# Kernel optimization log

Measured on AMD Instinct MI355X. Metric: run time of the kernel, lower is better.

Reference implementation:

```python
import jax, jax.numpy as jnp
import numpy as np

B, F, D, H = 256, 128, 512, 8
HD = D // H
SPARSITY = 0.5
KVAL = max(1, int(F * SPARSITY))  # 64


def setup_inputs() -> dict:
    key = jax.random.key(0)
    ks = jax.random.split(key, 12)
    s = 0.02
    x = jax.random.normal(ks[0], (B, F, D), dtype=jnp.float32)
    Wq = jax.random.normal(ks[1], (D, D), dtype=jnp.float32) * s
    bq = jnp.zeros((D,), jnp.float32)
    Wk = jax.random.normal(ks[2], (D, D), dtype=jnp.float32) * s
    bk = jnp.zeros((D,), jnp.float32)
    Wv = jax.random.normal(ks[3], (D, D), dtype=jnp.float32) * s
    bv = jnp.zeros((D,), jnp.float32)
    Wo = jax.random.normal(ks[4], (D, D), dtype=jnp.float32) * s
    bo = jnp.zeros((D,), jnp.float32)
    # correlation prior init: 0.5 * exp(-0.1 * |i-j|)
    idx = jnp.arange(F, dtype=jnp.float32)
    corr_prior = 0.5 * jnp.exp(-0.1 * jnp.abs(idx[:, None] - idx[None, :]))
    feat_imp = jnp.ones((F,), jnp.float32)
    # price_vol_detector: Linear(2D->D), SiLU, Linear(D->1), Sigmoid
    W1 = jax.random.normal(ks[5], (2 * D, D), dtype=jnp.float32) * s
    b1 = jnp.zeros((D,), jnp.float32)
    W2 = jax.random.normal(ks[6], (D, 1), dtype=jnp.float32) * s
    b2 = jnp.zeros((1,), jnp.float32)
    return {"x": x, "Wq": Wq, "bq": bq, "Wk": Wk, "bk": bk, "Wv": Wv, "bv": bv,
            "Wo": Wo, "bo": bo, "corr_prior": corr_prior, "feat_imp": feat_imp,
            "W1": W1, "b1": b1, "W2": W2, "b2": b2}


def reference(x, Wq, bq, Wk, bk, Wv, bv, Wo, bo, corr_prior, feat_imp, W1, b1, W2, b2):
    def split_heads(t):  # [B,F,D] -> [B,H,F,HD]
        return t.reshape(B, F, H, HD).transpose(0, 2, 1, 3)

    q = split_heads(x @ Wq + bq)
    k = split_heads(x @ Wk + bk)
    v = split_heads(x @ Wv + bv)

    scores = jnp.einsum('bhqd,bhkd->bhqk', q, k) / np.sqrt(HD).astype(np.float32)

    # correlation prior * pairwise feature importance
    imp = feat_imp[:, None] * feat_imp[None, :]          # [F,F]
    scores = scores + (corr_prior * imp)[None, None]     # broadcast to [B,H,F,F]

    # price-vol gating (n_features >= 2)
    mid = F // 2
    price = x[:, :mid].mean(axis=1)                      # [B,D]
    vol = x[:, mid:].mean(axis=1)                        # [B,D]
    combined = jnp.concatenate([price, vol], axis=1)     # [B,2D]
    h = jax.nn.silu(combined @ W1 + b1)
    pv = jax.nn.sigmoid(h @ W2 + b2).reshape(B, 1, 1, 1)  # [B,1,1,1]
    fidx = jnp.arange(F)
    pv_mask = ((fidx[:, None] < mid) ^ (fidx[None, :] < mid)).astype(scores.dtype)  # [F,F]
    scores = scores + pv * pv_mask[None, None] * 0.5

    # per-row top-k sparsification (same for all heads; vectorized over heads)
    topk_vals = jax.lax.top_k(scores, KVAL)[0]           # [B,H,F,KVAL]
    thresh = topk_vals[..., -1:]                          # kth largest per row
    scores = jnp.where(scores < thresh, jnp.float32(-1e9), scores)

    attn = jax.nn.softmax(scores, axis=-1)               # dropout: eval mode (identity)
    out = jnp.einsum('bhqk,bhkd->bhqd', attn, v)         # [B,H,F,HD]
    out = out.transpose(0, 2, 1, 3).reshape(B, F, D)     # merge heads
    return out @ Wo + bo
```

## Files before the change

kernel.cpp:

```cpp
#include <hip/hip_runtime.h>
#include <hip/hip_bf16.h>
#include <cstdint>

#define B_ 256
#define F_ 128
#define D_ 512
#define H_ 8
#define KVAL_ 64

typedef unsigned short ushort_t;
typedef __attribute__((ext_vector_type(8))) short short8;
typedef __attribute__((ext_vector_type(4))) float floatx4;
typedef __attribute__((ext_vector_type(2))) float floatx2;
typedef __attribute__((ext_vector_type(2))) double doublex2;

__device__ __forceinline__ unsigned f2ord32(float f) {
  unsigned b = __float_as_uint(f);
  return (b & 0x80000000u) ? ~b : (b | 0x80000000u);
}

__device__ __forceinline__ unsigned long long f2ord64(double s) {
  unsigned long long b = (unsigned long long)__double_as_longlong(s);
  return (b & 0x8000000000000000ull) ? ~b : (b | 0x8000000000000000ull);
}

__device__ __forceinline__ float bcast(float v, int l) {
  return __uint_as_float(__builtin_amdgcn_readlane(__float_as_uint(v), l));
}

__device__ __forceinline__ ushort_t f2bf(float f) {
  __hip_bfloat16 h = __float2bfloat16(f);
  return *reinterpret_cast<ushort_t*>(&h);
}
__device__ __forceinline__ float bf2f(ushort_t u) {
  __hip_bfloat16 h = *reinterpret_cast<__hip_bfloat16*>(&u);
  return __bfloat162float(h);
}

__global__ __launch_bounds__(256) void pv_kernel(
    const float* __restrict__ x, const float* __restrict__ W1,
    const float* __restrict__ b1, const float* __restrict__ W2,
    const float* __restrict__ b2, double* __restrict__ pv) {
  __shared__ double comb[1024];
  __shared__ double red[4];
  int b = blockIdx.x, t = threadIdx.x;
  {
    const float* xb = x + (size_t)b * (F_ * D_) + 2 * t;
    double p0 = 0.0, p1 = 0.0, v0 = 0.0, v1 = 0.0;
#pragma unroll 8
    for (int f = 0; f < 64; ++f) {
      floatx2 xp = *(const floatx2*)(xb + (size_t)f * D_);
      floatx2 xv = *(const floatx2*)(xb + (size_t)(f + 64) * D_);
      p0 += (double)xp[0];
      p1 += (double)xp[1];
      v0 += (double)xv[0];
      v1 += (double)xv[1];
    }
    comb[2 * t] = p0 * (1.0 / 64.0);
    comb[2 * t + 1] = p1 * (1.0 / 64.0);
    comb[512 + 2 * t] = v0 * (1.0 / 64.0);
    comb[512 + 2 * t + 1] = v1 * (1.0 / 64.0);
  }
  __syncthreads();
  double a0 = (double)b1[2 * t], a1 = (double)b1[2 * t + 1];
  const float* wp = W1 + 2 * t;
#pragma unroll 8
  for (int k = 0; k < 1024; ++k) {
    double c = comb[k];
    floatx2 wv = *(const floatx2*)(wp + (size_t)k * 512);
    a0 += c * (double)wv[0];
    a1 += c * (double)wv[1];
  }
  double h0 = a0 / (1.0 + exp(-a0));
  double h1 = a1 / (1.0 + exp(-a1));
  double part = h0 * (double)W2[2 * t] + h1 * (double)W2[2 * t + 1];
  for (int off = 32; off; off >>= 1) part += __shfl_xor(part, off);
  int lane = t & 63, w = t >> 6;
  if (lane == 0) red[w] = part;
  __syncthreads();
  if (t == 0) {
    double tot = red[0] + red[1] + red[2] + red[3] + (double)b2[0];
    pv[b] = 1.0 / (1.0 + exp(-tot));
  }
}

__global__ __launch_bounds__(256) void pack_wqk3_kernel(
    const float* __restrict__ Wq, const float* __restrict__ Wk,
    const float* __restrict__ bq, const float* __restrict__ bk,
    ushort_t* __restrict__ Wh, ushort_t* __restrict__ Wm,
    ushort_t* __restrict__ Wl, double* __restrict__ bqk) {
  int idx = blockIdx.x * 256 + threadIdx.x;
  int n = idx >> 9, k = idx & 511;
  float v = (n < 512) ? Wq[(size_t)k * 512 + n] : Wk[(size_t)k * 512 + (n - 512)];
  ushort_t h = f2bf(v);
  float r1 = v - bf2f(h);
  ushort_t m = f2bf(r1);
  ushort_t l = f2bf(r1 - bf2f(m));
  Wh[idx] = h;
  Wm[idx] = m;
  Wl[idx] = l;
  if (idx < 1024)
    bqk[idx] = (double)((idx < 512) ? bq[idx] : bk[idx - 512]);
}

__global__ __launch_bounds__(256) void pack_wt_kernel(
    const float* __restrict__ W, ushort_t* __restrict__ hiT,
    ushort_t* __restrict__ loT) {
  int i = blockIdx.x * 256 + threadIdx.x;
  int n = i >> 9, k = i & 511;
  float v = W[(size_t)k * 512 + n];
  ushort_t h = f2bf(v);
  hiT[i] = h;
  loT[i] = f2bf(v - bf2f(h));
}

__global__ __launch_bounds__(256) void xsplit3_kernel(
    const float* __restrict__ x, ushort_t* __restrict__ xh,
    ushort_t* __restrict__ xm, ushort_t* __restrict__ xl) {
  int i = blockIdx.x * 256 + threadIdx.x;
  const float* xp = x + (size_t)i * 8;
  floatx4 f0 = *(const floatx4*)xp;
  floatx4 f1 = *(const floatx4*)(xp + 4);
  short8 vh, vm, vl;
#pragma unroll
  for (int j = 0; j < 8; ++j) {
    float fv = (j < 4) ? f0[j] : f1[j - 4];
    ushort_t hb = f2bf(fv);
    float r1 = fv - bf2f(hb);
    ushort_t mb = f2bf(r1);
    ushort_t lb = f2bf(r1 - bf2f(mb));
    vh[j] = (short)hb;
    vm[j] = (short)mb;
    vl[j] = (short)lb;
  }
  *(short8*)&xh[(size_t)i * 8] = vh;
  *(short8*)&xm[(size_t)i * 8] = vm;
  *(short8*)&xl[(size_t)i * 8] = vl;
}

__global__ __launch_bounds__(256) void mfma_qk_v3(
    const ushort_t* __restrict__ Xh, const ushort_t* __restrict__ Xm,
    const ushort_t* __restrict__ Xl, const ushort_t* __restrict__ Wh,
    const ushort_t* __restrict__ Wm, const ushort_t* __restrict__ Wl,
    const double* __restrict__ bias, double* __restrict__ C) {
  __shared__ ushort_t As[3][128 * 40];
  __shared__ ushort_t Bs[3][128 * 40];
  int t = threadIdx.x;
  int lane = t & 63, w = t >> 6;
  int wm_ = w >> 1, wn = w & 1;
  int mrow = lane & 15, quad = lane >> 4;
  int m0 = blockIdx.y * 128, n0 = blockIdx.x * 128;
  floatx4 acc[4][4] = {};
  for (int kp = 0; kp < 16; ++kp) {
    int k0 = kp * 32;
    __syncthreads();
#pragma unroll
    for (int p = 0; p < 2; ++p) {
      int idx = p * 256 + t;
      int r = idx >> 2, c = (idx & 3) * 8;
      size_t aoff = (size_t)(m0 + r) * 512 + k0 + c;
      *(short8*)&As[0][r * 40 + c] = *(const short8*)(Xh + aoff);
      *(short8*)&As[1][r * 40 + c] = *(const short8*)(Xm + aoff);
      *(short8*)&As[2][r * 40 + c] = *(const short8*)(Xl + aoff);
      size_t boff = (size_t)(n0 + r) * 512 + k0 + c;
      *(short8*)&Bs[0][r * 40 + c] = *(const short8*)(Wh + boff);
      *(short8*)&Bs[1][r * 40 + c] = *(const short8*)(Wm + boff);
      *(short8*)&Bs[2][r * 40 + c] = *(const short8*)(Wl + boff);
    }
    __syncthreads();
#pragma unroll
    for (int sa = 0; sa < 3; ++sa) {
      short8 af[4];
#pragma unroll
      for (int mt = 0; mt < 4; ++mt)
        af[mt] = *(const short8*)&As[sa][(wm_ * 64 + mt * 16 + mrow) * 40 + quad * 8];
#pragma unroll
      for (int sb = 0; sb < 3; ++sb) {
        if (sa + sb > 2) continue;
        short8 bf[4];
#pragma unroll
        for (int nt = 0; nt < 4; ++nt)
          bf[nt] = *(const short8*)&Bs[sb][(wn * 64 + nt * 16 + mrow) * 40 + quad * 8];
#pragma unroll
        for (int mt = 0; mt < 4; ++mt)
#pragma unroll
          for (int nt = 0; nt < 4; ++nt)
            acc[mt][nt] = __builtin_amdgcn_mfma_f32_16x16x32_bf16(
                af[mt], bf[nt], acc[mt][nt], 0, 0, 0);
      }
    }
  }
#pragma unroll
  for (int nt = 0; nt < 4; ++nt) {
    int gn = n0 + wn * 64 + nt * 16 + mrow;
    double bb = bias[gn];
#pragma unroll
    for (int mt = 0; mt < 4; ++mt) {
      int gm = m0 + wm_ * 64 + mt * 16 + quad * 4;
#pragma unroll
      for (int rg = 0; rg < 4; ++rg)
        C[(size_t)(gm + rg) * 1024 + gn] = (double)acc[mt][nt][rg] + bb;
    }
  }
}

__global__ __launch_bounds__(256) void mfma_gemm_split(
    const float* __restrict__ A, const ushort_t* __restrict__ WhiT,
    const ushort_t* __restrict__ WloT, const float* __restrict__ bias,
    float* __restrict__ C) {
  __shared__ ushort_t As[128 * 40];
  __shared__ ushort_t Bs[128 * 40];
  int t = threadIdx.x;
  int lane = t & 63, w = t >> 6;
  int wm = w >> 1, wn = w & 1;
  int mrow = lane & 15, quad = lane >> 4;
  int m0 = blockIdx.y * 128, n0 = blockIdx.x * 128;
  floatx4 acc[4][4] = {};
  for (int kt = 0; kt < 48; ++kt) {
    int seg = kt >> 4;
    int k0 = (kt & 15) * 32;
    const ushort_t* Bseg = (seg == 1) ? WloT : WhiT;
    bool lo = (seg == 2);
    __syncthreads();
#pragma unroll
    for (int p = 0; p < 2; ++p) {
      int idx = p * 256 + t;
      int r = idx >> 2, c = idx & 3;
      const float* ap = A + (size_t)(m0 + r) * 512 + k0 + c * 8;
      floatx4 f0 = *(const floatx4*)ap;
      floatx4 f1 = *(const floatx4*)(ap + 4);
      short8 av;
#pragma unroll
      for (int j = 0; j < 8; ++j) {
        float fv = (j < 4) ? f0[j] : f1[j - 4];
        ushort_t hb = f2bf(fv);
        ushort_t ob = lo ? f2bf(fv - bf2f(hb)) : hb;
        av[j] = (short)ob;
      }
      *(short8*)&As[r * 40 + c * 8] = av;
      *(short8*)&Bs[r * 40 + c * 8] =
          *(const short8*)(Bseg + (size_t)(n0 + r) * 512 + k0 + c * 8);
    }
    __syncthreads();
    short8 af[4], bf8[4];
    int abase = (wm * 64 + mrow) * 40 + quad * 8;
    int bbase = (wn * 64 + mrow) * 40 + quad * 8;
#pragma unroll
    for (int i = 0; i < 4; ++i) {
      af[i] = *(const short8*)&As[abase + i * 640];
      bf8[i] = *(const short8*)&Bs[bbase + i * 640];
    }
#pragma unroll
    for (int mt = 0; mt < 4; ++mt)
#pragma unroll
      for (int nt = 0; nt < 4; ++nt)
        acc[mt][nt] = __builtin_amdgcn_mfma_f32_16x16x32_bf16(
            af[mt], bf8[nt], acc[mt][nt], 0, 0, 0);
  }
#pragma unroll
  for (int nt = 0; nt < 4; ++nt) {
    int gn = n0 + wn * 64 + nt * 16 + mrow;
    float bb = bias[gn];
#pragma unroll
    for (int mt = 0; mt < 4; ++mt) {
      int gm = m0 + wm * 64 + mt * 16 + quad * 4;
#pragma unroll
      for (int rg = 0; rg < 4; ++rg)
        C[(size_t)(gm + rg) * 512 + gn] = acc[mt][nt][rg] + bb;
    }
  }
}

__global__ __launch_bounds__(1024) void attn_kernel(
    const double* __restrict__ qk, const float* __restrict__ vbuf,
    const float* __restrict__ corr_prior, const float* __restrict__ feat_imp,
    const double* __restrict__ pv, float* __restrict__ attn_out, int b_off) {
  __shared__ double kT[64][128];
  __shared__ __align__(16) double qp[16][512];
  int bh = blockIdx.x;
  int b = bh >> 3, h = bh & 7;
  int t = threadIdx.x, lane = t & 63, w = t >> 6;
#pragma unroll
  for (int n = 0; n < 8; ++n) {
    int f = w + 16 * n;
    kT[lane][(f + lane) & 127] =
        qk[((size_t)(b * F_ + f)) * 1024 + 512 + h * 64 + lane];
  }
  __syncthreads();
  double pvb = pv[b_off + b] * 0.5;
  double fiA = (double)feat_imp[lane];
  double fiB = (double)feat_imp[64 + lane];
  const double SLOPE = 2.5e5;
  {
    int fb = 8 * w;
#pragma unroll
    for (int i = 0; i < 8; ++i)
      qp[w][i * 64 + lane] =
          qk[((size_t)(b * F_ + fb + i)) * 1024 + h * 64 + lane];
    double s0[8], s1[8];
#pragma unroll
    for (int i = 0; i < 8; ++i) {
      s0[i] = 0.0;
      s1[i] = 0.0;
    }
#pragma unroll 2
    for (int d = 0; d < 64; d += 2) {
      double kd0a = kT[d][(lane + d) & 127];
      double kd1a = kT[d][(lane + 64 + d) & 127];
      double kd0b = kT[d + 1][(lane + 1 + d) & 127];
      double kd1b = kT[d + 1][(lane + 65 + d) & 127];
#pragma unroll
      for (int i = 0; i < 8; ++i) {
        doublex2 q2 = *(const doublex2*)&qp[w][i * 64 + d];
        s0[i] += q2[0] * kd0a;
        s1[i] += q2[0] * kd1a;
        s0[i] += q2[1] * kd0b;
        s1[i] += q2[1] * kd1b;
      }
    }
    float p0s[8], p1s[8];
#pragma unroll
    for (int i = 0; i < 8; ++i) {
      int f = fb + i;
      double sa = s0[i], sb = s1[i];
      double fif = (double)feat_imp[f];
      double cp0 = (double)corr_prior[f * 128 + lane] * fif * fiA;
      double cp1 = (double)corr_prior[f * 128 + 64 + lane] * fif * fiB;
      double add0 = (f < 64) ? 0.0 : pvb;
      double add1 = (f < 64) ? pvb : 0.0;
      sa = sa * 0.125 + cp0 + add0;
      sb = sb * 0.125 + cp1 + add1;
      unsigned a0 = f2ord32((float)sa), a1 = f2ord32((float)sb), T = 0u;
      for (int bit = 31; bit >= 0; --bit) {
        unsigned cand = T | (1u << bit);
        int c = __popcll(__ballot(a0 >= cand)) + __popcll(__ballot(a1 >= cand));
        if (c >= KVAL_) T = cand;
      }
      int cnt_gt = __popcll(__ballot(a0 > T)) + __popcll(__ballot(a1 > T));
      int cnt_ge = __popcll(__ballot(a0 >= T)) + __popcll(__ballot(a1 >= T));
      int bsz = cnt_ge - cnt_gt;
      int r = KVAL_ - cnt_gt;
      double bmax = -1e300;
      if (a0 < T) bmax = sa;
      if (a1 < T && sb > bmax) bmax = sb;
      for (int off = 32; off; off >>= 1) bmax = fmax(bmax, __shfl_xor(bmax, off));
      double sT, sU;
      if (bsz == r) {
        double tmin = 1e300;
        if (a0 == T) tmin = sa;
        if (a1 == T && sb < tmin) tmin = sb;
        for (int off = 32; off; off >>= 1) tmin = fmin(tmin, __shfl_xor(tmin, off));
        sT = tmin;
        sU = bmax;
      } else {
        unsigned long long x0 = (a0 == T) ? f2ord64(sa) : 0ull;
        unsigned long long x1 = (a1 == T) ? f2ord64(sb) : 0ull;
        unsigned long long T64 = 0ull;
        for (int bit = 63; bit >= 0; --bit) {
          unsigned long long cand = T64 | (1ull << bit);
          int c = __popcll(__ballot(x0 >= cand)) + __popcll(__ballot(x1 >= cand));
          if (c >= r) T64 = cand;
        }
        double tv = -1e300, uv = bmax;
        if (x0 == T64) tv = sa;
        if (x1 == T64 && sb > tv) tv = sb;
        if (a0 == T && x0 < T64 && sa > uv) uv = sa;
        if (a1 == T && x1 < T64 && sb > uv) uv = sb;
        for (int off = 32; off; off >>= 1) {
          tv = fmax(tv, __shfl_xor(tv, off));
          uv = fmax(uv, __shfl_xor(uv, off));
        }
        sT = tv;
        sU = uv;
      }
      double mid = 0.5 * (sT + sU);
      double W0 = fmin(1.0, fmax(0.0, 0.5 + (sa - mid) * SLOPE));
      double W1v = fmin(1.0, fmax(0.0, 0.5 + (sb - mid) * SLOPE));
      double mm = fmax(sa, sb);
      for (int off = 32; off; off >>= 1) mm = fmax(mm, __shfl_xor(mm, off));
      float p0 = (float)W0 * expf((float)(sa - mm));
      float p1 = (float)W1v * expf((float)(sb - mm));
      float zz = p0 + p1;
      for (int off = 32; off; off >>= 1) zz += __shfl_xor(zz, off);
      float inv = 1.f / zz;
      p0s[i] = p0 * inv;
      p1s[i] = p1 * inv;
    }
    float* pp = (float*)qp[w];
#pragma unroll
    for (int i = 0; i < 8; ++i) {
      pp[i * 128 + lane] = p0s[i];
      pp[i * 128 + 64 + lane] = p1s[i];
    }
    const float* vb = vbuf + ((size_t)b * F_) * 512 + h * 64 + lane;
    float o[8] = {0.f, 0.f, 0.f, 0.f, 0.f, 0.f, 0.f, 0.f};
    float vj0 = vb[0], vj1 = vb[512];
    for (int j = 0; j < 128; j += 2) {
      float va = vj0, vbb = vj1;
      if (j + 2 < 128) {
        vj0 = vb[(size_t)(j + 2) * 512];
        vj1 = vb[(size_t)(j + 3) * 512];
      }
#pragma unroll
      for (int i = 0; i < 8; ++i) {
        floatx2 p2 = *(const floatx2*)&pp[i * 128 + j];
        o[i] += p2[0] * va;
        o[i] += p2[1] * vbb;
      }
    }
#pragma unroll
    for (int i = 0; i < 8; ++i)
      attn_out[((size_t)(b * F_ + fb + i)) * 512 + h * 64 + lane] = o[i];
  }
}

extern "C" void kernel_launch(void* const* d_in, const int* in_sizes, int n_in,
                              void* d_out, int out_size, void* d_ws,
                              size_t ws_size, hipStream_t stream) {
  const float* x = (const float*)d_in[0];
  const float* Wq = (const float*)d_in[1];
  const float* bq = (const float*)d_in[2];
  const float* Wk = (const float*)d_in[3];
  const float* bk = (const float*)d_in[4];
  const float* Wv = (const float*)d_in[5];
  const float* bv = (const float*)d_in[6];
  const float* Wo = (const float*)d_in[7];
  const float* bo = (const float*)d_in[8];
  const float* corr = (const float*)d_in[9];
  const float* fimp = (const float*)d_in[10];
  const float* W1 = (const float*)d_in[11];
  const float* b1 = (const float*)d_in[12];
  const float* W2 = (const float*)d_in[13];
  const float* b2 = (const float*)d_in[14];
  float* out = (float*)d_out;
  float* ws = (float*)d_ws;

  double* pv_hi = (double*)ws;
  double* bqk_hi = (double*)(ws + 512);
  ushort_t* WqkTh = (ushort_t*)(ws + 2560);
  ushort_t* WqkTm = (ushort_t*)(ws + 264704);
  ushort_t* WqkTl = (ushort_t*)(ws + 526848);
  ushort_t* WvhiT = (ushort_t*)(ws + 788992);
  ushort_t* WvloT = (ushort_t*)(ws + 920064);
  ushort_t* WohiT = (ushort_t*)(ws + 1051136);
  ushort_t* WoloT = (ushort_t*)(ws + 1182208);
  float* vbuf = ws + 1313280;
  float* attnb = ws + 18090496;
  double* qk = (double*)(ws + 34867712);
  const size_t head = 34867712;
  size_t ws_floats = ws_size / 4;
  int Bc = 8;
  for (int cand = 256; cand >= 8; cand >>= 1)
    if (head + (size_t)cand * 311296 <= ws_floats) { Bc = cand; break; }
  ushort_t* Xh = (ushort_t*)(ws + head + (size_t)Bc * 262144);
  ushort_t* Xm = Xh + (size_t)Bc * 65536;
  ushort_t* Xl = Xm + (size_t)Bc * 65536;

  hipLaunchKernelGGL(pv_kernel, dim3(B_), dim3(256), 0, stream,
                     x, W1, b1, W2, b2, pv_hi);
  hipLaunchKernelGGL(pack_wqk3_kernel, dim3(2048), dim3(256), 0, stream,
                     Wq, Wk, bq, bk, WqkTh, WqkTm, WqkTl, bqk_hi);
  hipLaunchKernelGGL(pack_wt_kernel, dim3(1024), dim3(256), 0, stream,
                     Wv, WvhiT, WvloT);
  hipLaunchKernelGGL(pack_wt_kernel, dim3(1024), dim3(256), 0, stream,
                     Wo, WohiT, WoloT);
  hipLaunchKernelGGL(mfma_gemm_split, dim3(4, 256), dim3(256), 0, stream,
                     x, WvhiT, WvloT, bv, vbuf);
  for (int b0 = 0; b0 < B_; b0 += Bc) {
    hipLaunchKernelGGL(xsplit3_kernel, dim3(Bc * 32), dim3(256), 0, stream,
                       x + (size_t)b0 * 65536, Xh, Xm, Xl);
    hipLaunchKernelGGL(mfma_qk_v3, dim3(8, Bc), dim3(256), 0, stream,
                       Xh, Xm, Xl, WqkTh, WqkTm, WqkTl, bqk_hi, qk);
    hipLaunchKernelGGL(attn_kernel, dim3(Bc * 8), dim3(1024), 0, stream,
                       qk, vbuf + (size_t)b0 * 65536, corr, fimp, pv_hi,
                       attnb + (size_t)b0 * 65536, b0);
  }
  hipLaunchKernelGGL(mfma_gemm_split, dim3(4, 256), dim3(256), 0, stream,
                     attnb, WohiT, WoloT, bo, out);
}
```

Measured before the change: 1.193 ms.

## Fuse split-bf16 GEMM passes and remap blocks across XCDs for locality

The V/O projection GEMM used to run three separate 16-step K sweeps (hi*hi, hi*lo, lo*hi), reloading A and B each pass. It now loads the hi and lo tiles of A and B once per K step and issues all three MFMA products from shared memory, cutting global loads and A-side bf16 conversion work. The QK GEMM, the projection GEMM and the attention kernel also switch to a 1D grid with a permutation that sends contiguous output tiles or batches to the same XCD (block index mod 8), aiming for better L2 reuse. The cost is twice the LDS per GEMM block, which may lower occupancy.

```diff
diff --git a/kernel.cpp b/kernel.cpp
--- a/kernel.cpp
+++ b/kernel.cpp
@@ -142,14 +142,16 @@
     const ushort_t* __restrict__ Xh, const ushort_t* __restrict__ Xm,
     const ushort_t* __restrict__ Xl, const ushort_t* __restrict__ Wh,
     const ushort_t* __restrict__ Wm, const ushort_t* __restrict__ Wl,
-    const double* __restrict__ bias, double* __restrict__ C) {
+    const double* __restrict__ bias, double* __restrict__ C, int nb) {
   __shared__ ushort_t As[3][128 * 40];
   __shared__ ushort_t Bs[3][128 * 40];
+  int s = blockIdx.x;
+  int o = (s & 7) * nb + (s >> 3);
+  int n0 = (o & 7) * 128, m0 = (o >> 3) * 128;
   int t = threadIdx.x;
   int lane = t & 63, w = t >> 6;
   int wm_ = w >> 1, wn = w & 1;
   int mrow = lane & 15, quad = lane >> 4;
-  int m0 = blockIdx.y * 128, n0 = blockIdx.x * 128;
   floatx4 acc[4][4] = {};
   for (int kp = 0; kp < 16; ++kp) {
     int k0 = kp * 32;
@@ -208,54 +210,79 @@
     const float* __restrict__ A, const ushort_t* __restrict__ WhiT,
     const ushort_t* __restrict__ WloT, const float* __restrict__ bias,
     float* __restrict__ C) {
-  __shared__ ushort_t As[128 * 40];
-  __shared__ ushort_t Bs[128 * 40];
+  __shared__ ushort_t Ah[128 * 40];
+  __shared__ ushort_t Al[128 * 40];
+  __shared__ ushort_t Bh[128 * 40];
+  __shared__ ushort_t Bl[128 * 40];
+  int s = blockIdx.x;
+  int o = (s & 7) * 128 + (s >> 3);
+  int n0 = (o & 3) * 128, m0 = (o >> 2) * 128;
   int t = threadIdx.x;
   int lane = t & 63, w = t >> 6;
   int wm = w >> 1, wn = w & 1;
   int mrow = lane & 15, quad = lane >> 4;
-  int m0 = blockIdx.y * 128, n0 = blockIdx.x * 128;
   floatx4 acc[4][4] = {};
-  for (int kt = 0; kt < 48; ++kt) {
-    int seg = kt >> 4;
-    int k0 = (kt & 15) * 32;
-    const ushort_t* Bseg = (seg == 1) ? WloT : WhiT;
-    bool lo = (seg == 2);
+  for (int kp = 0; kp < 16; ++kp) {
+    int k0 = kp * 32;
     __syncthreads();
 #pragma unroll
     for (int p = 0; p < 2; ++p) {
       int idx = p * 256 + t;
-      int r = idx >> 2, c = idx & 3;
-      const float* ap = A + (size_t)(m0 + r) * 512 + k0 + c * 8;
+      int r = idx >> 2, c = (idx & 3) * 8;
+      const float* ap = A + (size_t)(m0 + r) * 512 + k0 + c;
       floatx4 f0 = *(const floatx4*)ap;
       floatx4 f1 = *(const floatx4*)(ap + 4);
-      short8 av;
+      short8 vh, vl;
 #pragma unroll
       for (int j = 0; j < 8; ++j) {
         float fv = (j < 4) ? f0[j] : f1[j - 4];
         ushort_t hb = f2bf(fv);
-        ushort_t ob = lo ? f2bf(fv - bf2f(hb)) : hb;
-        av[j] = (short)ob;
-      }
-      *(short8*)&As[r * 40 + c * 8] = av;
-      *(short8*)&Bs[r * 40 + c * 8] =
-          *(const short8*)(Bseg + (size_t)(n0 + r) * 512 + k0 + c * 8);
+        vh[j] = (short)hb;
+        vl[j] = (short)f2bf(fv - bf2f(hb));
+      }
+      *(short8*)&Ah[r * 40 + c] = vh;
+      *(short8*)&Al[r * 40 + c] = vl;
+      size_t boff = (size_t)(n0 + r) * 512 + k0 + c;
+      *(short8*)&Bh[r * 40 + c] = *(const short8*)(WhiT + boff);
+      *(short8*)&Bl[r * 40 + c] = *(const short8*)(WloT + boff);
     }
     __syncthreads();
-    short8 af[4], bf8[4];
     int abase = (wm * 64 + mrow) * 40 + quad * 8;
     int bbase = (wn * 64 + mrow) * 40 + quad * 8;
+    short8 ah[4], bh[4];
 #pragma unroll
     for (int i = 0; i < 4; ++i) {
-      af[i] = *(const short8*)&As[abase + i * 640];
-      bf8[i] = *(const short8*)&Bs[bbase + i * 640];
+      ah[i] = *(const short8*)&Ah[abase + i * 640];
+      bh[i] = *(const short8*)&Bh[bbase + i * 640];
     }
 #pragma unroll
     for (int mt = 0; mt < 4; ++mt)
 #pragma unroll
       for (int nt = 0; nt < 4; ++nt)
         acc[mt][nt] = __builtin_amdgcn_mfma_f32_16x16x32_bf16(
-            af[mt], bf8[nt], acc[mt][nt], 0, 0, 0);
+            ah[mt], bh[nt], acc[mt][nt], 0, 0, 0);
+    {
+      short8 al[4];
+#pragma unroll
+      for (int i = 0; i < 4; ++i) al[i] = *(const short8*)&Al[abase + i * 640];
+#pragma unroll
+      for (int mt = 0; mt < 4; ++mt)
+#pragma unroll
+        for (int nt = 0; nt < 4; ++nt)
+          acc[mt][nt] = __builtin_amdgcn_mfma_f32_16x16x32_bf16(
+              al[mt], bh[nt], acc[mt][nt], 0, 0, 0);
+    }
+    {
+      short8 bl[4];
+#pragma unroll
+      for (int i = 0; i < 4; ++i) bl[i] = *(const short8*)&Bl[bbase + i * 640];
+#pragma unroll
+      for (int mt = 0; mt < 4; ++mt)
+#pragma unroll
+        for (int nt = 0; nt < 4; ++nt)
+          acc[mt][nt] = __builtin_amdgcn_mfma_f32_16x16x32_bf16(
+              ah[mt], bl[nt], acc[mt][nt], 0, 0, 0);
+    }
   }
 #pragma unroll
   for (int nt = 0; nt < 4; ++nt) {
@@ -274,11 +301,13 @@
 __global__ __launch_bounds__(1024) void attn_kernel(
     const double* __restrict__ qk, const float* __restrict__ vbuf,
     const float* __restrict__ corr_prior, const float* __restrict__ feat_imp,
-    const double* __restrict__ pv, float* __restrict__ attn_out, int b_off) {
+    const double* __restrict__ pv, float* __restrict__ attn_out, int b_off,
+    int nb) {
   __shared__ double kT[64][128];
   __shared__ __align__(16) double qp[16][512];
-  int bh = blockIdx.x;
-  int b = bh >> 3, h = bh & 7;
+  int s = blockIdx.x;
+  int o = (s & 7) * nb + (s >> 3);
+  int b = o >> 3, h = o & 7;
   int t = threadIdx.x, lane = t & 63, w = t >> 6;
 #pragma unroll
   for (int n = 0; n < 8; ++n) {
@@ -393,7 +422,7 @@
       pp[i * 128 + 64 + lane] = p1s[i];
     }
     const float* vb = vbuf + ((size_t)b * F_) * 512 + h * 64 + lane;
-    float o[8] = {0.f, 0.f, 0.f, 0.f, 0.f, 0.f, 0.f, 0.f};
+    float o8[8] = {0.f, 0.f, 0.f, 0.f, 0.f, 0.f, 0.f, 0.f};
     float vj0 = vb[0], vj1 = vb[512];
     for (int j = 0; j < 128; j += 2) {
       float va = vj0, vbb = vj1;
@@ -404,13 +433,13 @@
 #pragma unroll
       for (int i = 0; i < 8; ++i) {
         floatx2 p2 = *(const floatx2*)&pp[i * 128 + j];
-        o[i] += p2[0] * va;
-        o[i] += p2[1] * vbb;
+        o8[i] += p2[0] * va;
+        o8[i] += p2[1] * vbb;
       }
     }
 #pragma unroll
     for (int i = 0; i < 8; ++i)
-      attn_out[((size_t)(b * F_ + fb + i)) * 512 + h * 64 + lane] = o[i];
+      attn_out[((size_t)(b * F_ + fb + i)) * 512 + h * 64 + lane] = o8[i];
   }
 }
 
@@ -464,17 +493,17 @@
                      Wv, WvhiT, WvloT);
   hipLaunchKernelGGL(pack_wt_kernel, dim3(1024), dim3(256), 0, stream,
                      Wo, WohiT, WoloT);
-  hipLaunchKernelGGL(mfma_gemm_split, dim3(4, 256), dim3(256), 0, stream,
+  hipLaunchKernelGGL(mfma_gemm_split, dim3(1024), dim3(256), 0, stream,
                      x, WvhiT, WvloT, bv, vbuf);
   for (int b0 = 0; b0 < B_; b0 += Bc) {
     hipLaunchKernelGGL(xsplit3_kernel, dim3(Bc * 32), dim3(256), 0, stream,
                        x + (size_t)b0 * 65536, Xh, Xm, Xl);
-    hipLaunchKernelGGL(mfma_qk_v3, dim3(8, Bc), dim3(256), 0, stream,
-                       Xh, Xm, Xl, WqkTh, WqkTm, WqkTl, bqk_hi, qk);
+    hipLaunchKernelGGL(mfma_qk_v3, dim3(8 * Bc), dim3(256), 0, stream,
+                       Xh, Xm, Xl, WqkTh, WqkTm, WqkTl, bqk_hi, qk, Bc);
     hipLaunchKernelGGL(attn_kernel, dim3(Bc * 8), dim3(1024), 0, stream,
                        qk, vbuf + (size_t)b0 * 65536, corr, fimp, pv_hi,
-                       attnb + (size_t)b0 * 65536, b0);
-  }
-  hipLaunchKernelGGL(mfma_gemm_split, dim3(4, 256), dim3(256), 0, stream,
+                       attnb + (size_t)b0 * 65536, b0, Bc);
+  }
+  hipLaunchKernelGGL(mfma_gemm_split, dim3(1024), dim3(256), 0, stream,
                      attnb, WohiT, WoloT, bo, out);
 }
```

New measurement: 1.048 ms. 1.14x faster.
